# Optimization experiments

Measured on AMD Instinct MI355X. Metric: run time of the kernel, lower is better.

## Reference

```python
import jax, jax.numpy as jnp
import numpy as np

N_NODES = 100000


def _gcn_conv(x, row, col, W, b, num_nodes):
    """PyG GCNConv: symmetric normalization with self-loops, then linear.
    row/col already include self-loops. x: [N, d_in], W: [d_in, d_out]."""
    xw = x @ W  # [N, d_out]
    ones = jnp.ones(row.shape[0], dtype=x.dtype)
    deg = jax.ops.segment_sum(ones, col, num_segments=num_nodes)  # in-degree incl self-loop
    deg_inv_sqrt = jnp.where(deg > 0, jax.lax.rsqrt(jnp.maximum(deg, 1e-12)), 0.0)
    norm = deg_inv_sqrt[row] * deg_inv_sqrt[col]  # [E]
    msgs = xw[row] * norm[:, None]  # gather + scale, [E, d_out]
    out = jax.ops.segment_sum(msgs, col, num_segments=num_nodes)  # scatter-add
    return out + b


def _add_self_loops(edge_index, num_nodes):
    loop = jnp.arange(num_nodes, dtype=edge_index.dtype)
    row = jnp.concatenate([edge_index[0], loop])
    col = jnp.concatenate([edge_index[1], loop])
    return row, col


def setup_inputs() -> dict:
    key = jax.random.key(0)
    k_x, k_e, k_w1, k_b1, k_w2, k_b2 = jax.random.split(key, 6)
    in_dim, hidden_dim, out_dim = 64, 64, 32
    n_edges = 1600000
    x = jax.random.normal(k_x, (N_NODES, in_dim), dtype=jnp.float32)
    edge_index = jax.random.randint(k_e, (2, n_edges), 0, N_NODES, dtype=jnp.int64)
    # Glorot init like PyG's GCNConv linear weights
    s1 = float(np.sqrt(6.0 / (in_dim + hidden_dim)))
    s2 = float(np.sqrt(6.0 / (hidden_dim + out_dim)))
    W1 = jax.random.uniform(k_w1, (in_dim, hidden_dim), minval=-s1, maxval=s1, dtype=jnp.float32)
    b1 = jnp.zeros((hidden_dim,), dtype=jnp.float32)
    W2 = jax.random.uniform(k_w2, (hidden_dim, out_dim), minval=-s2, maxval=s2, dtype=jnp.float32)
    b2 = jnp.zeros((out_dim,), dtype=jnp.float32)
    return {"x": x, "edge_index": edge_index, "W1": W1, "b1": b1, "W2": W2, "b2": b2}


def reference(x, edge_index, W1, b1, W2, b2):
    row, col = _add_self_loops(edge_index, N_NODES)
    h = jax.nn.relu(_gcn_conv(x, row, col, W1, b1, N_NODES))
    out = _gcn_conv(h, row, col, W2, b2, N_NODES)
    return out
```

## Files before the change

kernel.cpp:

```cpp
#include <hip/hip_runtime.h>
#include <type_traits>

#define NN 100000
#define FB_SH 10
#define FB_N  1024
#define NFB   98
#define NBLK  256
#define BH_TOT (NFB * NBLK)

static __device__ __forceinline__ unsigned short f2bf(float f) {
    unsigned u = __float_as_uint(f);
    u += 0x7fffu + ((u >> 16) & 1u);
    return (unsigned short)(u >> 16);
}
static __device__ __forceinline__ float bf2f(unsigned short h) {
    return __uint_as_float(((unsigned)h) << 16);
}


__global__ __launch_bounds__(256) void k_hist1(const int* __restrict__ coli,
                                               int* __restrict__ bhist, int E, int chunk) {
    __shared__ int h[NFB];
    for (int i = threadIdx.x; i < NFB; i += 256) h[i] = 0;
    __syncthreads();
    int bk = blockIdx.x;
    int beg = bk * chunk, end = min(E, beg + chunk);
    for (int e = beg + threadIdx.x * 4; e < end; e += 1024) {
        if (e + 4 <= end) {
            int4 c = *(const int4*)&coli[e];
            atomicAdd(&h[c.x >> FB_SH], 1);
            atomicAdd(&h[c.y >> FB_SH], 1);
            atomicAdd(&h[c.z >> FB_SH], 1);
            atomicAdd(&h[c.w >> FB_SH], 1);
        } else {
            for (int t = e; t < end; ++t) atomicAdd(&h[coli[t] >> FB_SH], 1);
        }
    }
    __syncthreads();
    for (int i = threadIdx.x; i < NFB; i += 256)
        bhist[i * NBLK + bk] = h[i];
}

__global__ __launch_bounds__(1024) void k_scanA(int* __restrict__ a,
                                                int* __restrict__ blksum, int n) {
    __shared__ int sh[1024];
    int i = blockIdx.x * 1024 + threadIdx.x;
    int v = (i < n) ? a[i] : 0;
    sh[threadIdx.x] = v;
    __syncthreads();
    #pragma unroll
    for (int d = 1; d < 1024; d <<= 1) {
        int t = (threadIdx.x >= d) ? sh[threadIdx.x - d] : 0;
        __syncthreads();
        sh[threadIdx.x] += t;
        __syncthreads();
    }
    if (i < n) a[i] = sh[threadIdx.x] - v;
    if (threadIdx.x == 1023) blksum[blockIdx.x] = sh[1023];
}

__global__ __launch_bounds__(256) void k_scanC(int* __restrict__ a,
                                               const int* __restrict__ blksum,
                                               int nbs, int n,
                                               int* __restrict__ off, int E) {
    __shared__ int pre[32];
    if (threadIdx.x < 32) pre[threadIdx.x] = (threadIdx.x < nbs) ? blksum[threadIdx.x] : 0;
    __syncthreads();
    if (threadIdx.x == 0) {
        int s = 0;
        for (int b = 0; b < nbs; ++b) { int t = pre[b]; pre[b] = s; s += t; }
    }
    __syncthreads();
    int i = blockIdx.x * 256 + threadIdx.x;
    if (i < n) a[i] += pre[i >> 10];
    if (i == 0) off[NN] = E;
}

__global__ __launch_bounds__(256) void k_bin2(
    const int* __restrict__ rowi, const int* __restrict__ coli,
    const int* __restrict__ bbase, unsigned int* __restrict__ cbin, int E, int chunk)
{
    __shared__ int cur[NFB];
    int bk = blockIdx.x;
    for (int i = threadIdx.x; i < NFB; i += 256) cur[i] = bbase[i * NBLK + bk];
    __syncthreads();
    int beg = bk * chunk, end = min(E, beg + chunk);
    for (int e = beg + threadIdx.x * 4; e < end; e += 1024) {
        if (e + 4 <= end) {
            int4 c = *(const int4*)&coli[e];
            int4 r = *(const int4*)&rowi[e];
            int b0 = c.x >> FB_SH, b1 = c.y >> FB_SH, b2 = c.z >> FB_SH, b3 = c.w >> FB_SH;
            unsigned v0 = ((unsigned)r.x << FB_SH) | (unsigned)(c.x & (FB_N - 1));
            unsigned v1 = ((unsigned)r.y << FB_SH) | (unsigned)(c.y & (FB_N - 1));
            unsigned v2 = ((unsigned)r.z << FB_SH) | (unsigned)(c.z & (FB_N - 1));
            unsigned v3 = ((unsigned)r.w << FB_SH) | (unsigned)(c.w & (FB_N - 1));
            cbin[atomicAdd(&cur[b0], 1)] = v0;
            cbin[atomicAdd(&cur[b1], 1)] = v1;
            cbin[atomicAdd(&cur[b2], 1)] = v2;
            cbin[atomicAdd(&cur[b3], 1)] = v3;
        } else {
            for (int t = e; t < end; ++t) {
                int col = coli[t], row = rowi[t];
                int b = col >> FB_SH;
                unsigned val = ((unsigned)row << FB_SH) | (unsigned)(col & (FB_N - 1));
                cbin[atomicAdd(&cur[b], 1)] = val;
            }
        }
    }
}

__global__ __launch_bounds__(1024) void k_csr(
    const unsigned int* __restrict__ cbin, const int* __restrict__ bbase,
    int* __restrict__ off, float* __restrict__ dinv,
    int* __restrict__ srcs, int n, int E)
{
    __shared__ int hist[FB_N];
    __shared__ int wsum[16];
    int b = blockIdx.x;
    int beg = bbase[b * NBLK];
    int end = (b + 1 < NFB) ? bbase[(b + 1) * NBLK] : E;
    int tid = threadIdx.x;
    hist[tid] = 0;
    __syncthreads();
    int beg4 = min((beg + 3) & ~3, end);
    int end4 = max(end & ~3, beg4);
    int nhead = beg4 - beg;
    int ntail = end - end4;
    if (tid < nhead) atomicAdd(&hist[cbin[beg + tid] & (FB_N - 1)], 1);
    if (tid >= 4 && tid < 4 + ntail) atomicAdd(&hist[cbin[end4 + tid - 4] & (FB_N - 1)], 1);
    for (int e = beg4 + tid * 4; e < end4; e += 4096) {
        uint4 c = *(const uint4*)&cbin[e];
        atomicAdd(&hist[c.x & (FB_N - 1)], 1);
        atomicAdd(&hist[c.y & (FB_N - 1)], 1);
        atomicAdd(&hist[c.z & (FB_N - 1)], 1);
        atomicAdd(&hist[c.w & (FB_N - 1)], 1);
    }
    __syncthreads();
    int v = hist[tid];
    int lane = tid & 63;
    int wid  = tid >> 6;
    int incl = v;
    #pragma unroll
    for (int d = 1; d < 64; d <<= 1) {
        int t = __shfl_up(incl, d, 64);
        if (lane >= d) incl += t;
    }
    if (lane == 63) wsum[wid] = incl;
    __syncthreads();
    if (wid == 0) {
        int ws = (lane < 16) ? wsum[lane] : 0;
        int wincl = ws;
        #pragma unroll
        for (int d = 1; d < 16; d <<= 1) {
            int t = __shfl_up(wincl, d, 64);
            if (lane >= d) wincl += t;
        }
        if (lane < 16) wsum[lane] = wincl - ws;
    }
    __syncthreads();
    int excl = wsum[wid] + incl - v;
    int node = (b << FB_SH) + tid;
    if (node < n) {
        off[node]  = beg + excl;
        dinv[node] = rsqrtf((float)(v + 1));
    }
    __syncthreads();
    hist[tid] = excl;
    __syncthreads();
    if (tid < nhead) {
        unsigned pv = cbin[beg + tid];
        srcs[beg + atomicAdd(&hist[pv & (FB_N - 1)], 1)] = (int)(pv >> FB_SH);
    }
    if (tid >= 4 && tid < 4 + ntail) {
        unsigned pv = cbin[end4 + tid - 4];
        srcs[beg + atomicAdd(&hist[pv & (FB_N - 1)], 1)] = (int)(pv >> FB_SH);
    }
    for (int e = beg4 + tid * 4; e < end4; e += 4096) {
        uint4 c = *(const uint4*)&cbin[e];
        srcs[beg + atomicAdd(&hist[c.x & (FB_N - 1)], 1)] = (int)(c.x >> FB_SH);
        srcs[beg + atomicAdd(&hist[c.y & (FB_N - 1)], 1)] = (int)(c.y >> FB_SH);
        srcs[beg + atomicAdd(&hist[c.z & (FB_N - 1)], 1)] = (int)(c.z >> FB_SH);
        srcs[beg + atomicAdd(&hist[c.w & (FB_N - 1)], 1)] = (int)(c.w >> FB_SH);
    }
}

template<int DOUT, typename TIN>
__global__ __launch_bounds__(256) void k_gemm_scale(
    const TIN* __restrict__ X, const float* __restrict__ W,
    const float* __restrict__ dinv, unsigned short* __restrict__ Ybf, int n)
{
    constexpr int TPR = DOUT / 4;
    constexpr int R   = 256 / TPR;
    __shared__ float sW[64 * DOUT];
    __shared__ float sX[R * 64];

    for (int i = threadIdx.x; i < 16 * DOUT; i += 256)
        *(float4*)&sW[i * 4] = *(const float4*)&W[i * 4];
    int r0 = blockIdx.x * R;
    for (int i = threadIdx.x; i < R * 16; i += 256) {
        int lr  = i >> 4;
        int c4i = (i & 15) * 4;
        int r = r0 + lr;
        float4 v;
        if (r < n) {
            if constexpr (std::is_same<TIN, float>::value) {
                v = *(const float4*)&X[(size_t)r * 64 + c4i];
            } else {
                ushort4 u = *(const ushort4*)&X[(size_t)r * 64 + c4i];
                v = make_float4(bf2f(u.x), bf2f(u.y), bf2f(u.z), bf2f(u.w));
            }
        } else v = make_float4(0.f, 0.f, 0.f, 0.f);
        *(float4*)&sX[lr * 64 + c4i] = v;
    }
    __syncthreads();

    int lr  = threadIdx.x / TPR;
    int c4  = (threadIdx.x % TPR) * 4;
    int row = r0 + lr;
    const float* xr = &sX[lr * 64];
    float4 acc = make_float4(0.f, 0.f, 0.f, 0.f);
    #pragma unroll
    for (int k = 0; k < 64; ++k) {
        float xv = xr[k];
        const float* wr = &sW[k * DOUT + c4];
        acc.x = fmaf(xv, wr[0], acc.x);
        acc.y = fmaf(xv, wr[1], acc.y);
        acc.z = fmaf(xv, wr[2], acc.z);
        acc.w = fmaf(xv, wr[3], acc.w);
    }
    if (row < n) {
        float s = dinv[row];
        ushort4 o;
        o.x = f2bf(acc.x * s);
        o.y = f2bf(acc.y * s);
        o.z = f2bf(acc.z * s);
        o.w = f2bf(acc.w * s);
        *(ushort4*)&Ybf[(size_t)row * DOUT + c4] = o;
    }
}

__global__ __launch_bounds__(256) void k_agg64(
    const unsigned short* __restrict__ Ybf, const int* __restrict__ off,
    const int* __restrict__ srcs, const float* __restrict__ dinv,
    const float* __restrict__ bias, unsigned short* __restrict__ O, int n)
{
    int node = blockIdx.x * 4 + (threadIdx.x >> 6);
    if (node >= n) return;
    int l  = threadIdx.x & 63;
    int h  = l >> 5;
    int ch = (l & 31) * 2;
    int beg = off[node], end = off[node + 1];
    float a0 = 0.f, a1 = 0.f;
    int j = beg;
    for (; j + 16 <= end; j += 16) {
        #pragma unroll
        for (int k = 0; k < 8; ++k) {
            int src = srcs[j + 2 * k + h];
            ushort2 u = *(const ushort2*)&Ybf[(size_t)src * 64 + ch];
            a0 += bf2f(u.x); a1 += bf2f(u.y);
        }
    }
    for (; j + 2 <= end; j += 2) {
        int src = srcs[j + h];
        ushort2 u = *(const ushort2*)&Ybf[(size_t)src * 64 + ch];
        a0 += bf2f(u.x); a1 += bf2f(u.y);
    }
    if (h == 0) {
        if (j < end) {
            int src = srcs[j];
            ushort2 u = *(const ushort2*)&Ybf[(size_t)src * 64 + ch];
            a0 += bf2f(u.x); a1 += bf2f(u.y);
        }
        ushort2 u = *(const ushort2*)&Ybf[(size_t)node * 64 + ch];
        a0 += bf2f(u.x); a1 += bf2f(u.y);
    }
    a0 += __shfl_xor(a0, 32, 64);
    a1 += __shfl_xor(a1, 32, 64);
    if (h == 0) {
        float d = dinv[node];
        float o0 = fmaxf(fmaf(d, a0, bias[ch]),     0.f);
        float o1 = fmaxf(fmaf(d, a1, bias[ch + 1]), 0.f);
        ushort2 o;
        o.x = f2bf(o0);
        o.y = f2bf(o1);
        *(ushort2*)&O[(size_t)node * 64 + ch] = o;
    }
}

__global__ __launch_bounds__(256) void k_agg32(
    const unsigned short* __restrict__ Ybf, const int* __restrict__ off,
    const int* __restrict__ srcs, const float* __restrict__ dinv,
    const float* __restrict__ bias, float* __restrict__ O, int n)
{
    int node = blockIdx.x * 4 + (threadIdx.x >> 6);
    if (node >= n) return;
    int l  = threadIdx.x & 63;
    int q  = l >> 4;
    int ch = (l & 15) * 2;
    int beg = off[node], end = off[node + 1];
    float a0 = 0.f, a1 = 0.f;
    int j = beg;
    for (; j + 16 <= end; j += 16) {
        #pragma unroll
        for (int k = 0; k < 4; ++k) {
            int src = srcs[j + 4 * k + q];
            ushort2 u = *(const ushort2*)&Ybf[(size_t)src * 32 + ch];
            a0 += bf2f(u.x); a1 += bf2f(u.y);
        }
    }
    for (; j + 4 <= end; j += 4) {
        int src = srcs[j + q];
        ushort2 u = *(const ushort2*)&Ybf[(size_t)src * 32 + ch];
        a0 += bf2f(u.x); a1 += bf2f(u.y);
    }
    if (q < end - j) {
        int src = srcs[j + q];
        ushort2 u = *(const ushort2*)&Ybf[(size_t)src * 32 + ch];
        a0 += bf2f(u.x); a1 += bf2f(u.y);
    }
    if (q == 0) {
        ushort2 u = *(const ushort2*)&Ybf[(size_t)node * 32 + ch];
        a0 += bf2f(u.x); a1 += bf2f(u.y);
    }
    a0 += __shfl_xor(a0, 16, 64);
    a1 += __shfl_xor(a1, 16, 64);
    a0 += __shfl_xor(a0, 32, 64);
    a1 += __shfl_xor(a1, 32, 64);
    if (q == 0) {
        float d = dinv[node];
        float2 o;
        o.x = fmaf(d, a0, bias[ch]);
        o.y = fmaf(d, a1, bias[ch + 1]);
        *(float2*)&O[(size_t)node * 32 + ch] = o;
    }
}

extern "C" void kernel_launch(void* const* d_in, const int* in_sizes, int n_in,
                              void* d_out, int out_size, void* d_ws, size_t ws_size,
                              hipStream_t stream) {
    const float* x  = (const float*)d_in[0];
    const int*   ei = (const int*)d_in[1];
    const float* W1 = (const float*)d_in[2];
    const float* b1 = (const float*)d_in[3];
    const float* W2 = (const float*)d_in[4];
    const float* b2 = (const float*)d_in[5];
    float* out = (float*)d_out;

    const int n = NN;
    const int E = in_sizes[1] / 2;
    const int* rowi = ei;
    const int* coli = ei + E;
    const int chunk = (((E + NBLK - 1) / NBLK) + 3) & ~3;

    char* p = (char*)d_ws;
    auto alloc = [&p](size_t bytes) { char* q = p; p += (bytes + 255) & ~(size_t)255; return q; };
    int*   bhist  = (int*)alloc((size_t)BH_TOT * 4);
    int*   blksum = (int*)alloc(32 * 4);
    int*   off    = (int*)alloc((size_t)(n + 1) * 4);
    float* dinv   = (float*)alloc((size_t)n * 4);
    int*   srcs   = (int*)alloc((size_t)E * 4);
    unsigned short* Ybf1 = (unsigned short*)alloc((size_t)n * 64 * 2);
    unsigned short* Ybf2 = (unsigned short*)alloc((size_t)n * 32 * 2);
    unsigned short* Hbf  = (unsigned short*)alloc((size_t)n * 64 * 2);
    unsigned int* cbin = (unsigned int*)Hbf;

    k_hist1<<<NBLK, 256, 0, stream>>>(coli, bhist, E, chunk);
    int nbs = (BH_TOT + 1023) / 1024;
    k_scanA<<<nbs, 1024, 0, stream>>>(bhist, blksum, BH_TOT);
    k_scanC<<<(BH_TOT + 255) / 256, 256, 0, stream>>>(bhist, blksum, nbs, BH_TOT, off, E);
    k_bin2<<<NBLK, 256, 0, stream>>>(rowi, coli, bhist, cbin, E, chunk);
    k_csr<<<NFB, 1024, 0, stream>>>(cbin, bhist, off, dinv, srcs, n, E);

    k_gemm_scale<64, float><<<(n + 15) / 16, 256, 0, stream>>>(x, W1, dinv, Ybf1, n);
    k_agg64<<<(n + 3) / 4, 256, 0, stream>>>(Ybf1, off, srcs, dinv, b1, Hbf, n);

    k_gemm_scale<32, unsigned short><<<(n + 31) / 32, 256, 0, stream>>>(Hbf, W2, dinv, Ybf2, n);
    k_agg32<<<(n + 3) / 4, 256, 0, stream>>>(Ybf2, off, srcs, dinv, b2, out, n);
}
```

Measured before the change: 190.3 us.

## Fuse layer-2 weight multiply into the layer-1 aggregation epilogue

The second GCN layer's dense transform is folded into the layer-1 aggregation kernel. Each wavefront writes its ReLU'd hidden row to LDS and multiplies it by W2, which every block stages in shared memory. The result, pre-scaled by dinv, goes straight into the layer-2 bf16 buffer. This removes a kernel launch and the write and re-read of the hidden activation buffer. The cost is that every block reloads 8 KB of W2, and the extra LDS and compute may lower occupancy of the gather-bound kernel.

```diff
diff --git a/kernel.cpp b/kernel.cpp
--- a/kernel.cpp
+++ b/kernel.cpp
@@ -184,11 +184,11 @@
     }
 }
 
-template<int DOUT, typename TIN>
-__global__ __launch_bounds__(256) void k_gemm_scale(
-    const TIN* __restrict__ X, const float* __restrict__ W,
+__global__ __launch_bounds__(256) void k_gemm64(
+    const float* __restrict__ X, const float* __restrict__ W,
     const float* __restrict__ dinv, unsigned short* __restrict__ Ybf, int n)
 {
+    constexpr int DOUT = 64;
     constexpr int TPR = DOUT / 4;
     constexpr int R   = 256 / TPR;
     __shared__ float sW[64 * DOUT];
@@ -201,15 +201,8 @@
         int lr  = i >> 4;
         int c4i = (i & 15) * 4;
         int r = r0 + lr;
-        float4 v;
-        if (r < n) {
-            if constexpr (std::is_same<TIN, float>::value) {
-                v = *(const float4*)&X[(size_t)r * 64 + c4i];
-            } else {
-                ushort4 u = *(const ushort4*)&X[(size_t)r * 64 + c4i];
-                v = make_float4(bf2f(u.x), bf2f(u.y), bf2f(u.z), bf2f(u.w));
-            }
-        } else v = make_float4(0.f, 0.f, 0.f, 0.f);
+        float4 v = (r < n) ? *(const float4*)&X[(size_t)r * 64 + c4i]
+                           : make_float4(0.f, 0.f, 0.f, 0.f);
         *(float4*)&sX[lr * 64 + c4i] = v;
     }
     __syncthreads();
@@ -239,12 +232,20 @@
     }
 }
 
-__global__ __launch_bounds__(256) void k_agg64(
+__global__ __launch_bounds__(256) void k_agg64g(
     const unsigned short* __restrict__ Ybf, const int* __restrict__ off,
     const int* __restrict__ srcs, const float* __restrict__ dinv,
-    const float* __restrict__ bias, unsigned short* __restrict__ O, int n)
-{
-    int node = blockIdx.x * 4 + (threadIdx.x >> 6);
+    const float* __restrict__ bias, const float* __restrict__ W2,
+    unsigned short* __restrict__ Y2, int n)
+{
+    __shared__ float sW2[64 * 32];
+    __shared__ float sH[4][64];
+    for (int i = threadIdx.x; i < 512; i += 256)
+        *(float4*)&sW2[i * 4] = *(const float4*)&W2[i * 4];
+    __syncthreads();
+
+    int w    = threadIdx.x >> 6;
+    int node = blockIdx.x * 4 + w;
     if (node >= n) return;
     int l  = threadIdx.x & 63;
     int h  = l >> 5;
@@ -276,15 +277,23 @@
     }
     a0 += __shfl_xor(a0, 32, 64);
     a1 += __shfl_xor(a1, 32, 64);
+    float d = dinv[node];
     if (h == 0) {
-        float d = dinv[node];
-        float o0 = fmaxf(fmaf(d, a0, bias[ch]),     0.f);
-        float o1 = fmaxf(fmaf(d, a1, bias[ch + 1]), 0.f);
-        ushort2 o;
-        o.x = f2bf(o0);
-        o.y = f2bf(o1);
-        *(ushort2*)&O[(size_t)node * 64 + ch] = o;
-    }
+        float h0 = fmaxf(fmaf(d, a0, bias[ch]),     0.f);
+        float h1 = fmaxf(fmaf(d, a1, bias[ch + 1]), 0.f);
+        sH[w][ch]     = h0;
+        sH[w][ch + 1] = h1;
+    }
+    int jc = l & 31;
+    const float* hrow = &sH[w][h * 32];
+    const float* wcol = &sW2[(h * 32) * 32 + jc];
+    float acc2 = 0.f;
+    #pragma unroll
+    for (int k = 0; k < 32; ++k)
+        acc2 = fmaf(hrow[k], wcol[k * 32], acc2);
+    acc2 += __shfl_xor(acc2, 32, 64);
+    if (h == 0)
+        Y2[(size_t)node * 32 + jc] = f2bf(d * acc2);
 }
 
 __global__ __launch_bounds__(256) void k_agg32(
@@ -361,8 +370,7 @@
     int*   srcs   = (int*)alloc((size_t)E * 4);
     unsigned short* Ybf1 = (unsigned short*)alloc((size_t)n * 64 * 2);
     unsigned short* Ybf2 = (unsigned short*)alloc((size_t)n * 32 * 2);
-    unsigned short* Hbf  = (unsigned short*)alloc((size_t)n * 64 * 2);
-    unsigned int* cbin = (unsigned int*)Hbf;
+    unsigned int* cbin = (unsigned int*)Ybf1;
 
     k_hist1<<<NBLK, 256, 0, stream>>>(coli, bhist, E, chunk);
     int nbs = (BH_TOT + 1023) / 1024;
@@ -371,9 +379,9 @@
     k_bin2<<<NBLK, 256, 0, stream>>>(rowi, coli, bhist, cbin, E, chunk);
     k_csr<<<NFB, 1024, 0, stream>>>(cbin, bhist, off, dinv, srcs, n, E);
 
-    k_gemm_scale<64, float><<<(n + 15) / 16, 256, 0, stream>>>(x, W1, dinv, Ybf1, n);
-    k_agg64<<<(n + 3) / 4, 256, 0, stream>>>(Ybf1, off, srcs, dinv, b1, Hbf, n);
-
-    k_gemm_scale<32, unsigned short><<<(n + 31) / 32, 256, 0, stream>>>(Hbf, W2, dinv, Ybf2, n);
+    k_gemm64<<<(n + 15) / 16, 256, 0, stream>>>(x, W1, dinv, Ybf1, n);
+
+    k_agg64g<<<(n + 3) / 4, 256, 0, stream>>>(Ybf1, off, srcs, dinv, b1, W2, Ybf2, n);
+
     k_agg32<<<(n + 3) / 4, 256, 0, stream>>>(Ybf2, off, srcs, dinv, b2, out, n);
 }
```

Measured after the change: 184.2 us (median of 2 runs). 1.03x faster.
